# Kernel optimization log

Hardware: AMD Instinct MI355X
Metric: run time of the kernel (lower is better)

Reference implementation:

```python
import jax, jax.numpy as jnp
import numpy as np

INPUT_DIM = 64
OUTPUT_DIM = 128
KNN = 10          # hardcoded min(10, N) in source
RADIUS = 0.02     # density radius in source


def setup_inputs() -> dict:
    key = jax.random.key(0)
    k1, k2, k3, k4, k5, k6, k7 = jax.random.split(key, 7)
    B, N = 2, 8192
    points = jax.random.uniform(k1, (B, N, 3), dtype=jnp.float32)
    features = jax.random.normal(k2, (B, N, INPUT_DIM), dtype=jnp.float32)
    leaf_mask = jax.random.randint(k3, (B, N), 0, 2) > 0
    d_in = INPUT_DIM + 6
    s1 = 1.0 / np.sqrt(d_in)
    s2 = 1.0 / np.sqrt(OUTPUT_DIM)
    W1 = jax.random.uniform(k4, (d_in, OUTPUT_DIM), jnp.float32, -s1, s1)
    b1 = jax.random.uniform(k5, (OUTPUT_DIM,), jnp.float32, -s1, s1)
    W2 = jax.random.uniform(k6, (OUTPUT_DIM, OUTPUT_DIM), jnp.float32, -s2, s2)
    b2 = jax.random.uniform(k7, (OUTPUT_DIM,), jnp.float32, -s2, s2)
    return {"points": points, "features": features, "leaf_mask": leaf_mask,
            "W1": W1, "b1": b1, "W2": W2, "b2": b2}


def _leaf_geometry(points, mask):
    # points: [N,3], mask: [N] bool -> [N,6]
    mask_f = mask.astype(points.dtype)
    cnt = jnp.maximum(mask_f.sum(), 1.0)
    center = (points * mask_f[:, None]).sum(0) / cnt      # mean of masked points
    rel = points - center                                  # [N,3]
    dist_c = jnp.linalg.norm(rel, axis=1)                  # dist to leaf center
    rel_h = rel[:, 2]                                      # relative height
    horiz = jnp.linalg.norm(rel[:, :2], axis=1)            # horizontal distance
    # pairwise euclidean distances [N,N]; used only for thresholding and knn
    sq = jnp.sum(points * points, axis=1)
    d2 = sq[:, None] + sq[None, :] - 2.0 * (points @ points.T)
    dist = jax.lax.stop_gradient(jnp.sqrt(jnp.maximum(d2, 0.0)))
    density = jnp.sum((dist < RADIUS) & mask[None, :], axis=1).astype(points.dtype)
    # KNN (smallest distances, includes self) -> local PCA curvature
    _, idx = jax.lax.top_k(-dist, KNN)                     # [N,KNN]
    neighbors = points[idx]                                # [N,KNN,3]
    centered = neighbors - points[:, None, :]
    cov = jnp.einsum('nki,nkj->nij', centered, centered) / float(KNN)  # [N,3,3]
    ev = jnp.linalg.eigh(cov)[0]                           # ascending eigenvalues
    curv = ev[:, 0] / (ev[:, 2] + 1e-8)
    rad = jnp.arctan2(rel[:, 1], rel[:, 0])
    geom = jnp.stack([dist_c, rel_h, horiz, density, curv, rad], axis=1)
    # source returns zeros when mask is empty
    return jnp.where(mask_f.sum() > 0, geom, jnp.zeros_like(geom))


def reference(points, features, leaf_mask, W1, b1, W2, b2):
    geom = jax.vmap(_leaf_geometry)(points, leaf_mask)     # [B,N,6]
    combined = jnp.concatenate([features, geom], axis=-1)  # [B,N,input_dim+6]
    h = jax.nn.relu(combined @ W1 + b1)
    return jax.nn.relu(h @ W2 + b2)                        # [B,N,output_dim]
```

## Files before the change

kernel.cpp:

```cpp
#include <hip/hip_runtime.h>
#include <math.h>
#include <stdint.h>

#define B_SZ   2
#define N_PTS  8192
#define IN_DIM 64
#define D_IN   70
#define ODIM   128
#define NQ_ALL (B_SZ * N_PTS)
#define RADIUS_F 0.02f

#define GDIM  32
#define NCELL (GDIM * GDIM * GDIM)
#define HCELL 0.03125f

#define SUP     4
#define NSUP_AX 8
#define NSUPER  (NSUP_AX * NSUP_AX * NSUP_AX)
#define SCAP    352
#define LCAP    16
#define MAXROWS 100

typedef unsigned long long u64;

__device__ __forceinline__ void insert11(u64 (&best)[11], u64 key) {
#pragma unroll
  for (int j = 10; j >= 1; --j) {
    u64 hi = (best[j - 1] > key) ? best[j - 1] : key;
    best[j] = (best[j] < hi) ? best[j] : hi;
  }
  best[0] = (best[0] < key) ? best[0] : key;
}
__device__ __forceinline__ void insert10(u64 (&best)[10], u64 key) {
#pragma unroll
  for (int j = 9; j >= 1; --j) {
    u64 hi = (best[j - 1] > key) ? best[j - 1] : key;
    best[j] = (best[j] < hi) ? best[j] : hi;
  }
  best[0] = (best[0] < key) ? best[0] : key;
}

__device__ __forceinline__ float sq3(float x, float y, float z) {
  return __fadd_rn(__fadd_rn(__fmul_rn(x, x), __fmul_rn(y, y)), __fmul_rn(z, z));
}

__device__ __forceinline__ int cellOf(float v) {
  int c = (int)(v * 32.0f);
  return min(max(c, 0), GDIM - 1);
}

__device__ __forceinline__ void geom_epilogue(const float* __restrict__ P,
                                              const int (&idxs)[10], float dens,
                                              float px, float py, float pz,
                                              float4 ctr, float* __restrict__ g) {
  double c00 = 0, c01 = 0, c02 = 0, c11 = 0, c12 = 0, c22 = 0;
#pragma unroll
  for (int j = 0; j < 10; ++j) {
    const int idx = idxs[j];
    const float nx = P[3 * idx + 0], ny = P[3 * idx + 1], nz = P[3 * idx + 2];
    const float ex = __fsub_rn(nx, px);
    const float ey = __fsub_rn(ny, py);
    const float ez = __fsub_rn(nz, pz);
    c00 += (double)ex * ex; c01 += (double)ex * ey; c02 += (double)ex * ez;
    c11 += (double)ey * ey; c12 += (double)ey * ez; c22 += (double)ez * ez;
  }
  const double a00 = c00 / 10.0, a01 = c01 / 10.0, a02 = c02 / 10.0;
  const double a11 = c11 / 10.0, a12 = c12 / 10.0, a22 = c22 / 10.0;

  double p1 = a01 * a01 + a02 * a02 + a12 * a12;
  double qq = (a00 + a11 + a22) / 3.0;
  double p2 = (a00 - qq) * (a00 - qq) + (a11 - qq) * (a11 - qq) +
              (a22 - qq) * (a22 - qq) + 2.0 * p1;
  double ev0, ev2;
  if (p2 <= 1e-60) {
    ev0 = ev2 = qq;
  } else {
    double p = sqrt(p2 / 6.0);
    double invp = 1.0 / p;
    double b00 = (a00 - qq) * invp, b11 = (a11 - qq) * invp, b22 = (a22 - qq) * invp;
    double b01 = a01 * invp, b02 = a02 * invp, b12 = a12 * invp;
    double detB = b00 * (b11 * b22 - b12 * b12) - b01 * (b01 * b22 - b12 * b02) +
                  b02 * (b01 * b12 - b11 * b02);
    double r = 0.5 * detB;
    r = fmin(1.0, fmax(-1.0, r));
    double phi = acos(r) / 3.0;
    ev2 = qq + 2.0 * p * cos(phi);
    ev0 = qq + 2.0 * p * cos(phi + 2.0943951023931953);
  }
  const float curv = (float)(ev0 / (ev2 + 1e-08));

  const bool on = ctr.w > 0.0f;
  const float rx = __fsub_rn(px, ctr.x);
  const float ry = __fsub_rn(py, ctr.y);
  const float rz = __fsub_rn(pz, ctr.z);
  const float dist_c = sqrtf(sq3(rx, ry, rz));
  const float horiz  = sqrtf(__fadd_rn(__fmul_rn(rx, rx), __fmul_rn(ry, ry)));
  const float rad    = atan2f(ry, rx);

  g[0] = on ? dist_c : 0.0f;
  g[1] = on ? rz : 0.0f;
  g[2] = on ? horiz : 0.0f;
  g[3] = on ? dens : 0.0f;
  g[4] = on ? curv : 0.0f;
  g[5] = on ? rad : 0.0f;
}

__global__ __launch_bounds__(256) void k_build(const float* __restrict__ points,
                                               const int* __restrict__ mask,
                                               int* __restrict__ count,
                                               double* __restrict__ ctrAcc) {
  const int t = blockIdx.x * 256 + threadIdx.x;
  const int b = t >> 13;
  const int i = t & (N_PTS - 1);
  const float* P = points + (size_t)b * N_PTS * 3;
  const float x = P[3 * i + 0], y = P[3 * i + 1], z = P[3 * i + 2];
  atomicAdd(&count[b * NCELL + (cellOf(z) * GDIM + cellOf(y)) * GDIM + cellOf(x)], 1);

  const bool m = mask[b * N_PTS + i] != 0;
  double vx = m ? (double)x : 0.0, vy = m ? (double)y : 0.0;
  double vz = m ? (double)z : 0.0, vc = m ? 1.0 : 0.0;
#pragma unroll
  for (int s = 1; s < 64; s <<= 1) {
    vx += __shfl_xor(vx, s); vy += __shfl_xor(vy, s);
    vz += __shfl_xor(vz, s); vc += __shfl_xor(vc, s);
  }
  __shared__ double sh[4][4];
  const int w = threadIdx.x >> 6;
  if ((threadIdx.x & 63) == 0) { sh[0][w] = vx; sh[1][w] = vy; sh[2][w] = vz; sh[3][w] = vc; }
  __syncthreads();
  if (threadIdx.x == 0) {
    atomicAdd(&ctrAcc[b * 4 + 0], sh[0][0] + sh[0][1] + sh[0][2] + sh[0][3]);
    atomicAdd(&ctrAcc[b * 4 + 1], sh[1][0] + sh[1][1] + sh[1][2] + sh[1][3]);
    atomicAdd(&ctrAcc[b * 4 + 2], sh[2][0] + sh[2][1] + sh[2][2] + sh[2][3]);
    atomicAdd(&ctrAcc[b * 4 + 3], sh[3][0] + sh[3][1] + sh[3][2] + sh[3][3]);
  }
}

__global__ __launch_bounds__(1024) void k_scan(const int* __restrict__ count,
                                               int* __restrict__ start,
                                               int* __restrict__ cur,
                                               const double* __restrict__ ctrAcc,
                                               float* __restrict__ centerOut) {
  const int b = blockIdx.x;
  const int t = threadIdx.x;
  if (t == 0) {
    const float cf = (float)ctrAcc[b * 4 + 3];
    const float div = fmaxf(cf, 1.0f);
    centerOut[b * 4 + 0] = (float)ctrAcc[b * 4 + 0] / div;
    centerOut[b * 4 + 1] = (float)ctrAcc[b * 4 + 1] / div;
    centerOut[b * 4 + 2] = (float)ctrAcc[b * 4 + 2] / div;
    centerOut[b * 4 + 3] = (cf > 0.0f) ? 1.0f : 0.0f;
  }
  int c[32]; int sum = 0;
#pragma unroll
  for (int j = 0; j < 32; ++j) { c[j] = count[b * NCELL + t * 32 + j]; sum += c[j]; }
  __shared__ int s[1024];
  s[t] = sum;
  __syncthreads();
  for (int off = 1; off < 1024; off <<= 1) {
    int v = (t >= off) ? s[t - off] : 0;
    __syncthreads();
    if (t >= off) s[t] += v;
    __syncthreads();
  }
  int excl = (t > 0) ? s[t - 1] : 0;
#pragma unroll
  for (int j = 0; j < 32; ++j) {
    start[b * (NCELL + 1) + t * 32 + j] = excl;
    cur[b * NCELL + t * 32 + j] = excl;
    excl += c[j];
  }
  if (t == 1023) start[b * (NCELL + 1) + NCELL] = excl;
}

__global__ __launch_bounds__(256) void k_scatter(const float* __restrict__ points,
                                                 const int* __restrict__ mask,
                                                 int* __restrict__ cur,
                                                 float4* __restrict__ sorted) {
  const int t = blockIdx.x * 256 + threadIdx.x;
  const int b = t >> 13;
  const int i = t & (N_PTS - 1);
  const float* P = points + (size_t)b * N_PTS * 3;
  const float x = P[3 * i + 0], y = P[3 * i + 1], z = P[3 * i + 2];
  const int cell = (cellOf(z) * GDIM + cellOf(y)) * GDIM + cellOf(x);
  const int pos = atomicAdd(&cur[b * NCELL + cell], 1);
  const unsigned wb = (unsigned)i | ((mask[b * N_PTS + i] != 0) ? 0x80000000u : 0u);
  sorted[(size_t)b * N_PTS + pos] = make_float4(x, y, z, __uint_as_float(wb));
}

__global__ __launch_bounds__(128) void k_collect(const float* __restrict__ points,
                                                 const float4* __restrict__ sorted,
                                                 const int* __restrict__ start,
                                                 const float* __restrict__ center,
                                                 float* __restrict__ geom,
                                                 int* __restrict__ list,
                                                 int* __restrict__ listCnt,
                                                 float DENS_T) {
  const int b  = blockIdx.y;
  const int sc = blockIdx.x;
  const int sx = sc & 7, sy = (sc >> 3) & 7, sz = sc >> 6;
  const int tid = threadIdx.x;

  const int* ST = start + b * (NCELL + 1);
  const float4* SP = sorted + (size_t)b * N_PTS;

  const int x0 = SUP * sx, x1 = SUP * sx + SUP - 1;
  const int y0 = SUP * sy, y1 = SUP * sy + SUP - 1;
  const int z0 = SUP * sz, z1 = SUP * sz + SUP - 1;
  const int hx0 = max(x0 - 3, 0), hx1 = min(x1 + 3, GDIM - 1);
  const int hy0 = max(y0 - 3, 0), hy1 = min(y1 + 3, GDIM - 1);
  const int hz0 = max(z0 - 3, 0), hz1 = min(z1 + 3, GDIM - 1);
  const int yc = hy1 - hy0 + 1;
  const int R  = (hz1 - hz0 + 1) * yc;

  __shared__ int    rs[MAXROWS], rp[MAXROWS + 1];
  __shared__ int    qs_[16], qp_[17];
  __shared__ float4 pts4[SCAP];
  __shared__ u64    lbuf[128 * LCAP];

  if (tid < 64) {
    {
      int qlen = 0, qst = 0;
      if (tid < 16) {
        const int z = z0 + (tid >> 2), y = y0 + (tid & 3);
        const int base = (z * GDIM + y) * GDIM;
        qst  = ST[base + x0];
        qlen = ST[base + x1 + 1] - qst;
      }
      int inc = qlen;
      for (int off = 1; off < 64; off <<= 1) { int v = __shfl_up(inc, off); if (tid >= off) inc += v; }
      if (tid < 16) { qs_[tid] = qst; qp_[tid] = inc - qlen; }
      if (tid == 63) qp_[16] = inc;
    }
    {
      int len[2] = {0, 0}, st2[2] = {0, 0};
#pragma unroll
      for (int k = 0; k < 2; ++k) {
        const int r = tid * 2 + k;
        if (r < R) {
          const int z = hz0 + r / yc, y = hy0 + r % yc;
          const int base = (z * GDIM + y) * GDIM;
          st2[k] = ST[base + hx0];
          len[k] = ST[base + hx1 + 1] - st2[k];
        }
      }
      int sum = len[0] + len[1];
      int inc = sum;
      for (int off = 1; off < 64; off <<= 1) { int v = __shfl_up(inc, off); if (tid >= off) inc += v; }
      int exc = inc - sum;
#pragma unroll
      for (int k = 0; k < 2; ++k) {
        const int r = tid * 2 + k;
        if (r < R) { rs[r] = st2[k]; rp[r] = exc; }
        exc += len[k];
      }
      if (tid == 63) rp[R] = inc;
    }
  }
  __syncthreads();

  const int C    = rp[R];
  const int qtot = qp_[16];
  if (qtot == 0) return;

  if (C > SCAP) {
    for (int t = tid; t < qtot; t += 128) {
      int lo = 0, hi = 15;
      while (lo < hi) { const int mid = (lo + hi + 1) >> 1; if (qp_[mid] <= t) lo = mid; else hi = mid - 1; }
      const int qglob = qs_[lo] + (t - qp_[lo]);
      const int pos = atomicAdd(listCnt, 1);
      list[pos] = (b << 13) | qglob;
    }
    return;
  }

  for (int i = tid; i < C; i += 128) {
    int lo = 0, hi = R - 1;
    while (lo < hi) { const int mid = (lo + hi + 1) >> 1; if (rp[mid] <= i) lo = mid; else hi = mid - 1; }
    pts4[i] = SP[rs[lo] + (i - rp[lo])];
  }
  __syncthreads();

  const bool cxl = (x0 - 3 < 0), cxh = (x1 + 3 > GDIM - 1);
  const bool cyl = (y0 - 3 < 0), cyh = (y1 + 3 > GDIM - 1);
  const bool czl = (z0 - 3 < 0), czh = (z1 + 3 > GDIM - 1);

  const float4 ctr = reinterpret_cast<const float4*>(center)[b];
  const float* P = points + (size_t)b * N_PTS * 3;
  const int sub = tid & 7;
  const int gq  = tid >> 3;

  for (int q0 = 0; q0 < qtot; q0 += 16) {
    const int myq = q0 + gq;
    const bool act = (myq < qtot);
    const int mq = act ? myq : 0;
    int lo = 0, hi = 15;
    while (lo < hi) { const int mid = (lo + hi + 1) >> 1; if (qp_[mid] <= mq) lo = mid; else hi = mid - 1; }
    const int qglob = qs_[lo] + (mq - qp_[lo]);
    const float4 qp4 = SP[qglob];
    const int qidx = (int)(__float_as_uint(qp4.w) & 0x7FFFFFFFu);
    const float px = qp4.x, py = qp4.y, pz = qp4.z;
    const float sqq = sq3(px, py, pz);

    const float mxl = cxl ? 1e9f : __fsub_rn(px, (float)hx0 * HCELL);
    const float mxh = cxh ? 1e9f : __fsub_rn((float)(hx1 + 1) * HCELL, px);
    const float myl = cyl ? 1e9f : __fsub_rn(py, (float)hy0 * HCELL);
    const float myh = cyh ? 1e9f : __fsub_rn((float)(hy1 + 1) * HCELL, py);
    const float mzl = czl ? 1e9f : __fsub_rn(pz, (float)hz0 * HCELL);
    const float mzh = czh ? 1e9f : __fsub_rn((float)(hz1 + 1) * HCELL, pz);
    const float gr = fminf(fminf(fminf(mxl, mxh), fminf(myl, myh)), fminf(mzl, mzh));
    const float fx = 0.5f * (1.0f + fminf(fminf(px, 1.0f - px) * (1.0f / 0.0935f), 1.0f));
    const float fy = 0.5f * (1.0f + fminf(fminf(py, 1.0f - py) * (1.0f / 0.0935f), 1.0f));
    const float fz = 0.5f * (1.0f + fminf(fminf(pz, 1.0f - pz) * (1.0f / 0.0935f), 1.0f));
    const float rT = 0.0935f * cbrtf(1.0f / (fx * fy * fz));
    const float cR = fminf(gr, rT);
    const float cT2 = cR * cR;
    const float certR = cR * 0.999f;

    int cnt = 0;
    u64* myb = &lbuf[tid * LCAP];
#pragma unroll 2
    for (int j = sub; j < C; j += 8) {
      const float4 tp = pts4[j];
      const float sqc = sq3(tp.x, tp.y, tp.z);
      const float dot = __fmaf_rn(pz, tp.z, __fmaf_rn(py, tp.y, __fmul_rn(px, tp.x)));
      const float d2  = __fsub_rn(__fadd_rn(sqq, sqc), __fmul_rn(2.0f, dot));
      const float d2c = fmaxf(d2, 0.0f);
      if (d2c < cT2) {
        if (cnt < LCAP) {
          const unsigned wb = __float_as_uint(tp.w);
          myb[cnt] = ((u64)__float_as_uint(d2c) << 32)
                   | (u64)(((wb & 0x7FFFFFFFu) << 1) | (wb >> 31));
        }
        ++cnt;
      }
    }

    u64 best[11];
#pragma unroll
    for (int j = 0; j < 11; ++j) best[j] = ~0ull;
    float dens = 0.0f;
    const int m = min(cnt, LCAP);
    for (int i = 0; i < m; ++i) {
      const u64 e = myb[i];
      if ((e & 1ull) && __uint_as_float((unsigned)(e >> 32)) < DENS_T) dens += 1.0f;
      if (e < best[10]) insert11(best, e);
    }
    int cntg = cnt;
    int over = (cnt > LCAP) ? 1 : 0;
#pragma unroll
    for (int s = 1; s < 8; s <<= 1) {
      dens += __shfl_xor(dens, s);
      cntg += __shfl_xor(cntg, s);
      over |= __shfl_xor(over, s);
      u64 ok[11];
#pragma unroll
      for (int j = 0; j < 11; ++j) ok[j] = __shfl_xor(best[j], s);
#pragma unroll
      for (int j = 0; j < 11; ++j) {
        if (ok[j] < best[10]) insert11(best, ok[j]); else break;
      }
    }

    if (act && sub == 0) {
      const float dist9 = sqrtf(__uint_as_float((unsigned)(best[9] >> 32)));
      bool bad = (over != 0) || (cntg < 10) || !(dist9 < certR);
      if (cntg >= 11) {
        const float dist10 = sqrtf(__uint_as_float((unsigned)(best[10] >> 32)));
        bad = bad || (dist10 == dist9);
      }
      if (bad) {
        const int pos = atomicAdd(listCnt, 1);
        list[pos] = (b << 13) | qglob;
      } else {
        int idxs[10];
#pragma unroll
        for (int j = 0; j < 10; ++j) idxs[j] = (int)(((unsigned)best[j]) >> 1);
        geom_epilogue(P, idxs, dens, px, py, pz, ctr,
                      geom + ((size_t)b * N_PTS + qidx) * 6);
      }
    }
  }
}

__global__ __launch_bounds__(256) void k_wavefb(const float* __restrict__ points,
                                                const float4* __restrict__ sorted,
                                                const int* __restrict__ start,
                                                const float* __restrict__ center,
                                                float* __restrict__ geom,
                                                int* __restrict__ flags2,
                                                const int* __restrict__ list,
                                                const int* __restrict__ listCnt) {
  const int lane = threadIdx.x & 63;
  const int wid  = threadIdx.x >> 6;
  const int n = *listCnt;
  for (int it = blockIdx.x * 4 + wid; it < n; it += gridDim.x * 4) {
    const int e = list[it];
    const int b = e >> 13, qs = e & (N_PTS - 1);
    const float4* SP = sorted + (size_t)b * N_PTS;
    const int* ST = start + b * (NCELL + 1);
    const float4 qp = SP[qs];
    const int qidx = (int)(__float_as_uint(qp.w) & 0x7FFFFFFFu);
    const float px = qp.x, py = qp.y, pz = qp.z;
    const float sqq = sq3(px, py, pz);
    const int cx = cellOf(px), cy = cellOf(py), cz = cellOf(pz);
    const int xlo = max(cx - 8, 0), xhi = min(cx + 8, GDIM - 1);
    const int ylo = max(cy - 8, 0), yhi = min(cy + 8, GDIM - 1);
    const int zlo = max(cz - 8, 0), zhi = min(cz + 8, GDIM - 1);
    const int ycw = yhi - ylo + 1;
    const int Rw = (zhi - zlo + 1) * ycw;

    u64 best[10];
#pragma unroll
    for (int j = 0; j < 10; ++j) best[j] = ((u64)0x7F800000u << 32) | 0xFFFFFFFFu;
    float dens = 0.0f;

    for (int r = lane; r < Rw; r += 64) {
      const int z = zlo + r / ycw, y = ylo + r % ycw;
      const int base = (z * GDIM + y) * GDIM;
      const int j0 = ST[base + xlo], j1 = ST[base + xhi + 1];
      for (int j = j0; j < j1; ++j) {
        const float4 tp = SP[j];
        const unsigned wb = __float_as_uint(tp.w);
        const float sqc = sq3(tp.x, tp.y, tp.z);
        const float dot = __fmaf_rn(pz, tp.z, __fmaf_rn(py, tp.y, __fmul_rn(px, tp.x)));
        const float d2  = __fsub_rn(__fadd_rn(sqq, sqc), __fmul_rn(2.0f, dot));
        const float dist = sqrtf(fmaxf(d2, 0.0f));
        if ((dist < RADIUS_F) && (wb & 0x80000000u)) dens += 1.0f;
        const u64 key = ((u64)__float_as_uint(dist) << 32) | (wb & 0x7FFFFFFFu);
        if (key < best[9]) insert10(best, key);
      }
    }
#pragma unroll
    for (int s = 1; s < 64; s <<= 1) {
      dens += __shfl_xor(dens, s);
      u64 ok[10];
#pragma unroll
      for (int j = 0; j < 10; ++j) ok[j] = __shfl_xor(best[j], s);
#pragma unroll
      for (int j = 0; j < 10; ++j) {
        if (ok[j] < best[9]) insert10(best, ok[j]); else break;
      }
    }
    if (lane == 0) {
      const float dist9 = __uint_as_float((unsigned)(best[9] >> 32));
      if (dist9 < 0.2494f) {
        const float4 ctr = reinterpret_cast<const float4*>(center)[b];
        const float* P = points + (size_t)b * N_PTS * 3;
        int idxs[10];
#pragma unroll
        for (int j = 0; j < 10; ++j) idxs[j] = (int)(((unsigned)best[j]) & 0x7FFFFFFFu);
        geom_epilogue(P, idxs, dens, px, py, pz, ctr, geom + ((size_t)b * N_PTS + qidx) * 6);
      } else {
        flags2[b * N_PTS + qs] = 1;
      }
    }
  }
}

__global__ __launch_bounds__(256) void k_fallback(const float* __restrict__ points,
                                                  const float4* __restrict__ sorted,
                                                  const int* __restrict__ start,
                                                  const float* __restrict__ center,
                                                  float* __restrict__ geom,
                                                  const int* __restrict__ flags2) {
  const int b = blockIdx.y;
  const int qs = blockIdx.x * 256 + threadIdx.x;
  if (flags2[b * N_PTS + qs] == 0) return;
  const float4 qp = sorted[(size_t)b * N_PTS + qs];
  const unsigned qw = __float_as_uint(qp.w);
  const int qidx = (int)(qw & 0x7FFFFFFFu);

  const float px = qp.x, py = qp.y, pz = qp.z;
  const float sqq = sq3(px, py, pz);
  const int cx = cellOf(px), cy = cellOf(py), cz = cellOf(pz);

  const int* ST = start + b * (NCELL + 1);
  const float4* SP = sorted + (size_t)b * N_PTS;

  u64 best[10];
#pragma unroll
  for (int j = 0; j < 10; ++j) best[j] = ((u64)0x7F800000u << 32) | 0xFFFFFFFFu;
  float dens = 0.0f;

  for (int rho = 0; rho < GDIM; ++rho) {
    const int zlo = max(cz - rho, 0), zhi = min(cz + rho, GDIM - 1);
    const int ylo = max(cy - rho, 0), yhi = min(cy + rho, GDIM - 1);
    for (int z = zlo; z <= zhi; ++z) {
      const int adz = abs(z - cz);
      for (int y = ylo; y <= yhi; ++y) {
        const int ady = abs(y - cy);
        const int m2 = max(adz, ady);
        int ja, jb;
        int ja2 = 0, jb2 = 0;
        const int rowBase = (z * GDIM + y) * GDIM;
        if (m2 == rho) {
          const int xa = max(cx - rho, 0), xb = min(cx + rho, GDIM - 1);
          ja = ST[rowBase + xa]; jb = ST[rowBase + xb + 1];
        } else {
          ja = jb = 0;
          if (cx - rho >= 0)        { ja = ST[rowBase + cx - rho]; jb = ST[rowBase + cx - rho + 1]; }
          if (cx + rho <= GDIM - 1) { ja2 = ST[rowBase + cx + rho]; jb2 = ST[rowBase + cx + rho + 1]; }
        }
#pragma unroll 1
        for (int pass = 0; pass < 2; ++pass) {
          const int j0 = pass ? ja2 : ja;
          const int j1 = pass ? jb2 : jb;
          for (int j = j0; j < j1; ++j) {
            const float4 tp = SP[j];
            const unsigned wb = __float_as_uint(tp.w);
            const float sqc = sq3(tp.x, tp.y, tp.z);
            const float dot = __fmaf_rn(pz, tp.z, __fmaf_rn(py, tp.y, __fmul_rn(px, tp.x)));
            const float d2  = __fsub_rn(__fadd_rn(sqq, sqc), __fmul_rn(2.0f, dot));
            const float dist = sqrtf(fmaxf(d2, 0.0f));
            if ((dist < RADIUS_F) && (wb & 0x80000000u)) dens += 1.0f;
            const u64 key = ((u64)__float_as_uint(dist) << 32) | (wb & 0x7FFFFFFFu);
            if (key < best[9]) insert10(best, key);
          }
        }
      }
    }
    if (rho >= 1) {
      const float dist9 = __uint_as_float((unsigned)(best[9] >> 32));
      if (dist9 < (float)rho * HCELL * 0.999f) break;
    }
  }

  const float4 ctr = reinterpret_cast<const float4*>(center)[b];
  const float* P = points + (size_t)b * N_PTS * 3;
  int idxs[10];
#pragma unroll
  for (int j = 0; j < 10; ++j) idxs[j] = (int)(((unsigned)best[j]) & 0x7FFFFFFFu);
  geom_epilogue(P, idxs, dens, px, py, pz, ctr, geom + ((size_t)b * N_PTS + qidx) * 6);
}

__global__ __launch_bounds__(256) void k_mlp(const float* __restrict__ features,
                                             const float* __restrict__ geom,
                                             const float* __restrict__ W1,
                                             const float* __restrict__ b1,
                                             const float* __restrict__ W2,
                                             const float* __restrict__ b2,
                                             float* __restrict__ out) {
  __shared__ float Wbuf[ODIM * ODIM];
  __shared__ float A[64][71];
  __shared__ float H[64][133];
  const int tid = threadIdx.x;
  const int row0 = blockIdx.x * 64;

  {
    const int r = tid >> 2, f4 = (tid & 3) * 16;
#pragma unroll
    for (int j = 0; j < 4; ++j) {
      const float4 v = *reinterpret_cast<const float4*>(
          &features[(size_t)(row0 + r) * IN_DIM + f4 + j * 4]);
      A[r][f4 + 4 * j + 0] = v.x; A[r][f4 + 4 * j + 1] = v.y;
      A[r][f4 + 4 * j + 2] = v.z; A[r][f4 + 4 * j + 3] = v.w;
    }
  }
  for (int i = tid; i < 64 * 6; i += 256) {
    const int r = i / 6, k = i % 6;
    A[r][IN_DIM + k] = geom[(size_t)(row0 + r) * 6 + k];
  }
  for (int i = tid; i < D_IN * ODIM / 4; i += 256) {
    const float4 v = reinterpret_cast<const float4*>(W1)[i];
    Wbuf[4 * i + 0] = v.x; Wbuf[4 * i + 1] = v.y;
    Wbuf[4 * i + 2] = v.z; Wbuf[4 * i + 3] = v.w;
  }
  __syncthreads();

  const int rg = (tid >> 4) * 4;
  const int c  = (tid & 15) * 8;

  float acc[4][8];
#pragma unroll
  for (int i = 0; i < 4; ++i)
#pragma unroll
    for (int j = 0; j < 8; ++j) acc[i][j] = 0.0f;

#pragma unroll 2
  for (int k = 0; k < D_IN; ++k) {
    float a[4];
#pragma unroll
    for (int i = 0; i < 4; ++i) a[i] = A[rg + i][k];
    const float4 w0 = *reinterpret_cast<const float4*>(&Wbuf[k * ODIM + c]);
    const float4 w1 = *reinterpret_cast<const float4*>(&Wbuf[k * ODIM + c + 4]);
    const float w[8] = {w0.x, w0.y, w0.z, w0.w, w1.x, w1.y, w1.z, w1.w};
#pragma unroll
    for (int i = 0; i < 4; ++i)
#pragma unroll
      for (int j = 0; j < 8; ++j) acc[i][j] = fmaf(a[i], w[j], acc[i][j]);
  }
  __syncthreads();

  {
    const float4 bb0 = *reinterpret_cast<const float4*>(&b1[c]);
    const float4 bb1 = *reinterpret_cast<const float4*>(&b1[c + 4]);
    const float bb[8] = {bb0.x, bb0.y, bb0.z, bb0.w, bb1.x, bb1.y, bb1.z, bb1.w};
#pragma unroll
    for (int i = 0; i < 4; ++i) {
#pragma unroll
      for (int j = 0; j < 8; ++j) H[rg + i][c + j] = fmaxf(acc[i][j] + bb[j], 0.0f);
    }
  }
  for (int i = tid; i < ODIM * ODIM / 4; i += 256) {
    const float4 v = reinterpret_cast<const float4*>(W2)[i];
    Wbuf[4 * i + 0] = v.x; Wbuf[4 * i + 1] = v.y;
    Wbuf[4 * i + 2] = v.z; Wbuf[4 * i + 3] = v.w;
  }
  __syncthreads();

#pragma unroll
  for (int i = 0; i < 4; ++i)
#pragma unroll
    for (int j = 0; j < 8; ++j) acc[i][j] = 0.0f;

#pragma unroll 2
  for (int k = 0; k < ODIM; ++k) {
    float a[4];
#pragma unroll
    for (int i = 0; i < 4; ++i) a[i] = H[rg + i][k];
    const float4 w0 = *reinterpret_cast<const float4*>(&Wbuf[k * ODIM + c]);
    const float4 w1 = *reinterpret_cast<const float4*>(&Wbuf[k * ODIM + c + 4]);
    const float w[8] = {w0.x, w0.y, w0.z, w0.w, w1.x, w1.y, w1.z, w1.w};
#pragma unroll
    for (int i = 0; i < 4; ++i)
#pragma unroll
      for (int j = 0; j < 8; ++j) acc[i][j] = fmaf(a[i], w[j], acc[i][j]);
  }
  {
    const float4 bb0 = *reinterpret_cast<const float4*>(&b2[c]);
    const float4 bb1 = *reinterpret_cast<const float4*>(&b2[c + 4]);
    const float bb[8] = {bb0.x, bb0.y, bb0.z, bb0.w, bb1.x, bb1.y, bb1.z, bb1.w};
#pragma unroll
    for (int i = 0; i < 4; ++i) {
      const size_t row = (size_t)(row0 + rg + i);
      float4 o0 = make_float4(fmaxf(acc[i][0] + bb[0], 0.f), fmaxf(acc[i][1] + bb[1], 0.f),
                              fmaxf(acc[i][2] + bb[2], 0.f), fmaxf(acc[i][3] + bb[3], 0.f));
      float4 o1 = make_float4(fmaxf(acc[i][4] + bb[4], 0.f), fmaxf(acc[i][5] + bb[5], 0.f),
                              fmaxf(acc[i][6] + bb[6], 0.f), fmaxf(acc[i][7] + bb[7], 0.f));
      *reinterpret_cast<float4*>(&out[row * ODIM + c]) = o0;
      *reinterpret_cast<float4*>(&out[row * ODIM + c + 4]) = o1;
    }
  }
}

extern "C" void kernel_launch(void* const* d_in, const int* in_sizes, int n_in,
                              void* d_out, int out_size, void* d_ws, size_t ws_size,
                              hipStream_t stream) {
  const float* points   = (const float*)d_in[0];
  const float* features = (const float*)d_in[1];
  const int*   mask     = (const int*)d_in[2];
  const float* W1       = (const float*)d_in[3];
  const float* b1       = (const float*)d_in[4];
  const float* W2       = (const float*)d_in[5];
  const float* b2       = (const float*)d_in[6];
  float* out = (float*)d_out;

  const double Rd   = (double)0.02f;
  const double midd = Rd - ldexp(1.0, -30);
  const double Td   = midd * midd;
  float densT = (float)Td;
  if ((double)densT <= Td) densT = nextafterf(densT, 1.0f);

  char* w = (char*)d_ws;
  size_t off = 0;
  auto take = [&](size_t bytes) { char* p = w + off; off = (off + bytes + 255) & ~(size_t)255; return p; };
  float*  geomBuf   = (float*)take((size_t)NQ_ALL * 6 * 4);
  float*  centerBuf = (float*)take(2 * 16);
  char*   zero0     = (char*)take(0);
  int*    countBuf  = (int*)take((size_t)B_SZ * NCELL * 4);
  int*    flags2Buf = (int*)take((size_t)NQ_ALL * 4);
  int*    listCnt   = (int*)take(4);
  double* ctrAcc    = (double*)take((size_t)B_SZ * 4 * 8);
  char*   zero1     = (char*)take(0);
  int*    startBuf  = (int*)take((size_t)B_SZ * (NCELL + 1) * 4);
  int*    curBuf    = (int*)take((size_t)B_SZ * NCELL * 4);
  float4* sortedBuf = (float4*)take((size_t)B_SZ * N_PTS * 16);
  int*    listBuf   = (int*)take((size_t)NQ_ALL * 4);
  (void)ws_size;

  hipMemsetAsync(zero0, 0, (size_t)(zero1 - zero0), stream);
  k_build<<<NQ_ALL / 256, 256, 0, stream>>>(points, mask, countBuf, ctrAcc);
  k_scan<<<B_SZ, 1024, 0, stream>>>(countBuf, startBuf, curBuf, ctrAcc, centerBuf);
  k_scatter<<<NQ_ALL / 256, 256, 0, stream>>>(points, mask, curBuf, sortedBuf);
  k_collect<<<dim3(NSUPER, B_SZ), 128, 0, stream>>>(points, sortedBuf, startBuf, centerBuf,
                                                    geomBuf, listBuf, listCnt, densT);
  k_wavefb<<<512, 256, 0, stream>>>(points, sortedBuf, startBuf, centerBuf,
                                    geomBuf, flags2Buf, listBuf, listCnt);
  k_fallback<<<dim3(N_PTS / 256, B_SZ), 256, 0, stream>>>(points, sortedBuf, startBuf,
                                                          centerBuf, geomBuf, flags2Buf);
  k_mlp<<<NQ_ALL / 64, 256, 0, stream>>>(features, geomBuf, W1, b1, W2, b2, out);
}
```

Baseline: 206.4 us.

## Split collect supercells across four single-wave blocks with 16 lanes per query

Each supercell is now handled by four 64-thread blocks instead of one 128-thread block, and each block takes an interleaved subset of the query points. Each query is scanned by 16 lanes instead of 8. The per-lane candidate buffer shrinks to 12 entries with a padded stride, which is meant to cut shared-memory use and bank conflicts so more blocks fit per CU. The halo gather now copies contiguous rows directly instead of binary-searching per element. The cost is that every split block redundantly loads the full halo into shared memory, and the smaller buffer may push more queries onto the fallback path.

```diff
diff --git a/kernel.cpp b/kernel.cpp
--- a/kernel.cpp
+++ b/kernel.cpp
@@ -17,8 +17,10 @@
 #define SUP     4
 #define NSUP_AX 8
 #define NSUPER  (NSUP_AX * NSUP_AX * NSUP_AX)
+#define NSPLIT  4
 #define SCAP    352
-#define LCAP    16
+#define LCAP    12
+#define LSTR    (LCAP + 1)
 #define MAXROWS 100
 
 typedef unsigned long long u64;
@@ -188,18 +190,19 @@
   sorted[(size_t)b * N_PTS + pos] = make_float4(x, y, z, __uint_as_float(wb));
 }
 
-__global__ __launch_bounds__(128) void k_collect(const float* __restrict__ points,
-                                                 const float4* __restrict__ sorted,
-                                                 const int* __restrict__ start,
-                                                 const float* __restrict__ center,
-                                                 float* __restrict__ geom,
-                                                 int* __restrict__ list,
-                                                 int* __restrict__ listCnt,
-                                                 float DENS_T) {
-  const int b  = blockIdx.y;
-  const int sc = blockIdx.x;
+__global__ __launch_bounds__(64) void k_collect(const float* __restrict__ points,
+                                                const float4* __restrict__ sorted,
+                                                const int* __restrict__ start,
+                                                const float* __restrict__ center,
+                                                float* __restrict__ geom,
+                                                int* __restrict__ list,
+                                                int* __restrict__ listCnt,
+                                                float DENS_T) {
+  const int b    = blockIdx.y;
+  const int sc   = blockIdx.x / NSPLIT;
+  const int part = blockIdx.x % NSPLIT;
   const int sx = sc & 7, sy = (sc >> 3) & 7, sz = sc >> 6;
-  const int tid = threadIdx.x;
+  const int lane = threadIdx.x;
 
   const int* ST = start + b * (NCELL + 1);
   const float4* SP = sorted + (size_t)b * N_PTS;
@@ -216,46 +219,44 @@
   __shared__ int    rs[MAXROWS], rp[MAXROWS + 1];
   __shared__ int    qs_[16], qp_[17];
   __shared__ float4 pts4[SCAP];
-  __shared__ u64    lbuf[128 * LCAP];
-
-  if (tid < 64) {
-    {
-      int qlen = 0, qst = 0;
-      if (tid < 16) {
-        const int z = z0 + (tid >> 2), y = y0 + (tid & 3);
+  __shared__ u64    lbuf[64 * LSTR];
+
+  {
+    int qlen = 0, qst = 0;
+    if (lane < 16) {
+      const int z = z0 + (lane >> 2), y = y0 + (lane & 3);
+      const int base = (z * GDIM + y) * GDIM;
+      qst  = ST[base + x0];
+      qlen = ST[base + x1 + 1] - qst;
+    }
+    int inc = qlen;
+    for (int off = 1; off < 64; off <<= 1) { int v = __shfl_up(inc, off); if (lane >= off) inc += v; }
+    if (lane < 16) { qs_[lane] = qst; qp_[lane] = inc - qlen; }
+    if (lane == 63) qp_[16] = inc;
+  }
+  {
+    int len[2] = {0, 0}, st2[2] = {0, 0};
+#pragma unroll
+    for (int k = 0; k < 2; ++k) {
+      const int r = lane * 2 + k;
+      if (r < R) {
+        const int z = hz0 + r / yc, y = hy0 + r % yc;
         const int base = (z * GDIM + y) * GDIM;
-        qst  = ST[base + x0];
-        qlen = ST[base + x1 + 1] - qst;
-      }
-      int inc = qlen;
-      for (int off = 1; off < 64; off <<= 1) { int v = __shfl_up(inc, off); if (tid >= off) inc += v; }
-      if (tid < 16) { qs_[tid] = qst; qp_[tid] = inc - qlen; }
-      if (tid == 63) qp_[16] = inc;
-    }
-    {
-      int len[2] = {0, 0}, st2[2] = {0, 0};
-#pragma unroll
-      for (int k = 0; k < 2; ++k) {
-        const int r = tid * 2 + k;
-        if (r < R) {
-          const int z = hz0 + r / yc, y = hy0 + r % yc;
-          const int base = (z * GDIM + y) * GDIM;
-          st2[k] = ST[base + hx0];
-          len[k] = ST[base + hx1 + 1] - st2[k];
-        }
-      }
-      int sum = len[0] + len[1];
-      int inc = sum;
-      for (int off = 1; off < 64; off <<= 1) { int v = __shfl_up(inc, off); if (tid >= off) inc += v; }
-      int exc = inc - sum;
-#pragma unroll
-      for (int k = 0; k < 2; ++k) {
-        const int r = tid * 2 + k;
-        if (r < R) { rs[r] = st2[k]; rp[r] = exc; }
-        exc += len[k];
-      }
-      if (tid == 63) rp[R] = inc;
-    }
+        st2[k] = ST[base + hx0];
+        len[k] = ST[base + hx1 + 1] - st2[k];
+      }
+    }
+    int sum = len[0] + len[1];
+    int inc = sum;
+    for (int off = 1; off < 64; off <<= 1) { int v = __shfl_up(inc, off); if (lane >= off) inc += v; }
+    int exc = inc - sum;
+#pragma unroll
+    for (int k = 0; k < 2; ++k) {
+      const int r = lane * 2 + k;
+      if (r < R) { rs[r] = st2[k]; rp[r] = exc; }
+      exc += len[k];
+    }
+    if (lane == 63) rp[R] = inc;
   }
   __syncthreads();
 
@@ -264,20 +265,21 @@
   if (qtot == 0) return;
 
   if (C > SCAP) {
-    for (int t = tid; t < qtot; t += 128) {
-      int lo = 0, hi = 15;
-      while (lo < hi) { const int mid = (lo + hi + 1) >> 1; if (qp_[mid] <= t) lo = mid; else hi = mid - 1; }
-      const int qglob = qs_[lo] + (t - qp_[lo]);
-      const int pos = atomicAdd(listCnt, 1);
-      list[pos] = (b << 13) | qglob;
+    if (part == 0) {
+      for (int t = lane; t < qtot; t += 64) {
+        int lo = 0, hi = 15;
+        while (lo < hi) { const int mid = (lo + hi + 1) >> 1; if (qp_[mid] <= t) lo = mid; else hi = mid - 1; }
+        const int qglob = qs_[lo] + (t - qp_[lo]);
+        const int pos = atomicAdd(listCnt, 1);
+        list[pos] = (b << 13) | qglob;
+      }
     }
     return;
   }
 
-  for (int i = tid; i < C; i += 128) {
-    int lo = 0, hi = R - 1;
-    while (lo < hi) { const int mid = (lo + hi + 1) >> 1; if (rp[mid] <= i) lo = mid; else hi = mid - 1; }
-    pts4[i] = SP[rs[lo] + (i - rp[lo])];
+  for (int r = lane; r < R; r += 64) {
+    const int st = rs[r], base = rp[r], len = rp[r + 1] - base;
+    for (int t = 0; t < len; ++t) pts4[base + t] = SP[st + t];
   }
   __syncthreads();
 
@@ -287,10 +289,10 @@
 
   const float4 ctr = reinterpret_cast<const float4*>(center)[b];
   const float* P = points + (size_t)b * N_PTS * 3;
-  const int sub = tid & 7;
-  const int gq  = tid >> 3;
-
-  for (int q0 = 0; q0 < qtot; q0 += 16) {
+  const int sub = lane & 15;
+  const int gq  = lane >> 4;
+
+  for (int q0 = part * 4; q0 < qtot; q0 += NSPLIT * 4) {
     const int myq = q0 + gq;
     const bool act = (myq < qtot);
     const int mq = act ? myq : 0;
@@ -318,9 +320,9 @@
     const float certR = cR * 0.999f;
 
     int cnt = 0;
-    u64* myb = &lbuf[tid * LCAP];
+    u64* myb = &lbuf[lane * LSTR];
 #pragma unroll 2
-    for (int j = sub; j < C; j += 8) {
+    for (int j = sub; j < C; j += 16) {
       const float4 tp = pts4[j];
       const float sqc = sq3(tp.x, tp.y, tp.z);
       const float dot = __fmaf_rn(pz, tp.z, __fmaf_rn(py, tp.y, __fmul_rn(px, tp.x)));
@@ -349,7 +351,7 @@
     int cntg = cnt;
     int over = (cnt > LCAP) ? 1 : 0;
 #pragma unroll
-    for (int s = 1; s < 8; s <<= 1) {
+    for (int s = 1; s < 16; s <<= 1) {
       dens += __shfl_xor(dens, s);
       cntg += __shfl_xor(cntg, s);
       over |= __shfl_xor(over, s);
@@ -683,8 +685,9 @@
   k_build<<<NQ_ALL / 256, 256, 0, stream>>>(points, mask, countBuf, ctrAcc);
   k_scan<<<B_SZ, 1024, 0, stream>>>(countBuf, startBuf, curBuf, ctrAcc, centerBuf);
   k_scatter<<<NQ_ALL / 256, 256, 0, stream>>>(points, mask, curBuf, sortedBuf);
-  k_collect<<<dim3(NSUPER, B_SZ), 128, 0, stream>>>(points, sortedBuf, startBuf, centerBuf,
-                                                    geomBuf, listBuf, listCnt, densT);
+  k_collect<<<dim3(NSUPER * NSPLIT, B_SZ), 64, 0, stream>>>(points, sortedBuf, startBuf,
+                                                            centerBuf, geomBuf, listBuf,
+                                                            listCnt, densT);
   k_wavefb<<<512, 256, 0, stream>>>(points, sortedBuf, startBuf, centerBuf,
                                     geomBuf, flags2Buf, listBuf, listCnt);
   k_fallback<<<dim3(N_PTS / 256, B_SZ), 256, 0, stream>>>(points, sortedBuf, startBuf,
```

New measurement: 224.0 us. 8.6% more time.

## Split KNN geometry epilogue into separate kernel and use 32-bit top-k keys

Applied to the files above, without the earlier changes.

The collect kernel no longer runs the costly per-query geometry epilogue (covariance and eigen solve) on one lane in eight. Instead each 8-lane group cooperatively writes its 10 neighbour indices and density into a per-query record, and a new fully parallel k_geom2 kernel computes geometry from those records. The top-k merge now uses 32-bit distance keys rather than 64-bit ones, the per-thread candidate buffer in LDS gets a padded stride, and the scan loop unroll is raised. The cost is an extra kernel launch, a record buffer round-trip through global memory, and a second candidate pass to recover indices.

```diff
diff --git a/kernel.cpp b/kernel.cpp
--- a/kernel.cpp
+++ b/kernel.cpp
@@ -19,17 +19,18 @@
 #define NSUPER  (NSUP_AX * NSUP_AX * NSUP_AX)
 #define SCAP    352
 #define LCAP    16
+#define LSTR    17
 #define MAXROWS 100
 
 typedef unsigned long long u64;
 
-__device__ __forceinline__ void insert11(u64 (&best)[11], u64 key) {
+__device__ __forceinline__ void ins11u(unsigned (&best)[11], unsigned key) {
 #pragma unroll
   for (int j = 10; j >= 1; --j) {
-    u64 hi = (best[j - 1] > key) ? best[j - 1] : key;
-    best[j] = (best[j] < hi) ? best[j] : hi;
-  }
-  best[0] = (best[0] < key) ? best[0] : key;
+    unsigned hi = max(best[j - 1], key);
+    best[j] = min(best[j], hi);
+  }
+  best[0] = min(best[0], key);
 }
 __device__ __forceinline__ void insert10(u64 (&best)[10], u64 key) {
 #pragma unroll
@@ -188,11 +189,9 @@
   sorted[(size_t)b * N_PTS + pos] = make_float4(x, y, z, __uint_as_float(wb));
 }
 
-__global__ __launch_bounds__(128) void k_collect(const float* __restrict__ points,
-                                                 const float4* __restrict__ sorted,
+__global__ __launch_bounds__(128) void k_collect(const float4* __restrict__ sorted,
                                                  const int* __restrict__ start,
-                                                 const float* __restrict__ center,
-                                                 float* __restrict__ geom,
+                                                 int* __restrict__ recBuf,
                                                  int* __restrict__ list,
                                                  int* __restrict__ listCnt,
                                                  float DENS_T) {
@@ -216,7 +215,8 @@
   __shared__ int    rs[MAXROWS], rp[MAXROWS + 1];
   __shared__ int    qs_[16], qp_[17];
   __shared__ float4 pts4[SCAP];
-  __shared__ u64    lbuf[128 * LCAP];
+  __shared__ u64    lbuf[128 * LSTR];
+  __shared__ int    gslot[16][12];
 
   if (tid < 64) {
     {
@@ -268,6 +268,7 @@
       int lo = 0, hi = 15;
       while (lo < hi) { const int mid = (lo + hi + 1) >> 1; if (qp_[mid] <= t) lo = mid; else hi = mid - 1; }
       const int qglob = qs_[lo] + (t - qp_[lo]);
+      recBuf[((size_t)b * N_PTS + qglob) * 12 + 11] = 1;
       const int pos = atomicAdd(listCnt, 1);
       list[pos] = (b << 13) | qglob;
     }
@@ -285,10 +286,9 @@
   const bool cyl = (y0 - 3 < 0), cyh = (y1 + 3 > GDIM - 1);
   const bool czl = (z0 - 3 < 0), czh = (z1 + 3 > GDIM - 1);
 
-  const float4 ctr = reinterpret_cast<const float4*>(center)[b];
-  const float* P = points + (size_t)b * N_PTS * 3;
   const int sub = tid & 7;
   const int gq  = tid >> 3;
+  const int g   = tid >> 3;
 
   for (int q0 = 0; q0 < qtot; q0 += 16) {
     const int myq = q0 + gq;
@@ -298,7 +298,6 @@
     while (lo < hi) { const int mid = (lo + hi + 1) >> 1; if (qp_[mid] <= mq) lo = mid; else hi = mid - 1; }
     const int qglob = qs_[lo] + (mq - qp_[lo]);
     const float4 qp4 = SP[qglob];
-    const int qidx = (int)(__float_as_uint(qp4.w) & 0x7FFFFFFFu);
     const float px = qp4.x, py = qp4.y, pz = qp4.z;
     const float sqq = sq3(px, py, pz);
 
@@ -318,8 +317,8 @@
     const float certR = cR * 0.999f;
 
     int cnt = 0;
-    u64* myb = &lbuf[tid * LCAP];
-#pragma unroll 2
+    u64* myb = &lbuf[tid * LSTR];
+#pragma unroll 4
     for (int j = sub; j < C; j += 8) {
       const float4 tp = pts4[j];
       const float sqc = sq3(tp.x, tp.y, tp.z);
@@ -336,15 +335,16 @@
       }
     }
 
-    u64 best[11];
-#pragma unroll
-    for (int j = 0; j < 11; ++j) best[j] = ~0ull;
+    unsigned best[11];
+#pragma unroll
+    for (int j = 0; j < 11; ++j) best[j] = 0xFFFFFFFFu;
     float dens = 0.0f;
     const int m = min(cnt, LCAP);
     for (int i = 0; i < m; ++i) {
       const u64 e = myb[i];
-      if ((e & 1ull) && __uint_as_float((unsigned)(e >> 32)) < DENS_T) dens += 1.0f;
-      if (e < best[10]) insert11(best, e);
+      const unsigned d2u = (unsigned)(e >> 32);
+      if ((e & 1ull) && __uint_as_float(d2u) < DENS_T) dens += 1.0f;
+      if (d2u < best[10]) ins11u(best, d2u);
     }
     int cntg = cnt;
     int over = (cnt > LCAP) ? 1 : 0;
@@ -353,34 +353,71 @@
       dens += __shfl_xor(dens, s);
       cntg += __shfl_xor(cntg, s);
       over |= __shfl_xor(over, s);
-      u64 ok[11];
+      unsigned ok[11];
 #pragma unroll
       for (int j = 0; j < 11; ++j) ok[j] = __shfl_xor(best[j], s);
 #pragma unroll
       for (int j = 0; j < 11; ++j) {
-        if (ok[j] < best[10]) insert11(best, ok[j]); else break;
-      }
-    }
-
-    if (act && sub == 0) {
-      const float dist9 = sqrtf(__uint_as_float((unsigned)(best[9] >> 32)));
+        if (ok[j] < best[10]) ins11u(best, ok[j]); else break;
+      }
+    }
+
+    if (act) {
+      const unsigned T9 = best[9];
+      const float dist9 = sqrtf(__uint_as_float(T9));
       bool bad = (over != 0) || (cntg < 10) || !(dist9 < certR);
-      if (cntg >= 11) {
-        const float dist10 = sqrtf(__uint_as_float((unsigned)(best[10] >> 32)));
-        bad = bad || (dist10 == dist9);
-      }
-      if (bad) {
+      if (cntg >= 11) bad = bad || (sqrtf(__uint_as_float(best[10])) == dist9);
+      int* rec = recBuf + ((size_t)b * N_PTS + qglob) * 12;
+      if (!bad) {
+        int mc = 0;
+        for (int i = 0; i < m; ++i) if ((unsigned)(myb[i] >> 32) <= T9) ++mc;
+        int pre = mc;
+#pragma unroll
+        for (int off = 1; off < 8; off <<= 1) { int v = __shfl_up(pre, off); if (sub >= off) pre += v; }
+        int wp = pre - mc;
+        for (int i = 0; i < m; ++i) {
+          const u64 e = myb[i];
+          if ((unsigned)(e >> 32) <= T9) { gslot[g][min(wp, 11)] = (int)(((unsigned)e) >> 1); ++wp; }
+        }
+        __builtin_amdgcn_wave_barrier();
+        if (sub == 0) {
+          int4 r0 = make_int4(gslot[g][0], gslot[g][1], gslot[g][2], gslot[g][3]);
+          int4 r1 = make_int4(gslot[g][4], gslot[g][5], gslot[g][6], gslot[g][7]);
+          int4 r2 = make_int4(gslot[g][8], gslot[g][9], __float_as_int(dens), 0);
+          *reinterpret_cast<int4*>(rec + 0) = r0;
+          *reinterpret_cast<int4*>(rec + 4) = r1;
+          *reinterpret_cast<int4*>(rec + 8) = r2;
+        }
+        __builtin_amdgcn_wave_barrier();
+      } else if (sub == 0) {
+        rec[11] = 1;
         const int pos = atomicAdd(listCnt, 1);
         list[pos] = (b << 13) | qglob;
-      } else {
-        int idxs[10];
-#pragma unroll
-        for (int j = 0; j < 10; ++j) idxs[j] = (int)(((unsigned)best[j]) >> 1);
-        geom_epilogue(P, idxs, dens, px, py, pz, ctr,
-                      geom + ((size_t)b * N_PTS + qidx) * 6);
-      }
-    }
-  }
+      }
+    }
+  }
+}
+
+__global__ __launch_bounds__(256) void k_geom2(const float* __restrict__ points,
+                                               const float4* __restrict__ sorted,
+                                               const float* __restrict__ center,
+                                               const int* __restrict__ recBuf,
+                                               float* __restrict__ geom) {
+  const int t = blockIdx.x * 256 + threadIdx.x;
+  const int b = t >> 13;
+  const int qs = t & (N_PTS - 1);
+  const int* rec = recBuf + (size_t)t * 12;
+  if (rec[11] != 0) return;
+  const float4 qp = sorted[(size_t)b * N_PTS + qs];
+  const int qidx = (int)(__float_as_uint(qp.w) & 0x7FFFFFFFu);
+  int idxs[10];
+#pragma unroll
+  for (int j = 0; j < 10; ++j) idxs[j] = rec[j];
+  const float dens = __int_as_float(rec[10]);
+  const float4 ctr = reinterpret_cast<const float4*>(center)[b];
+  const float* P = points + (size_t)b * N_PTS * 3;
+  geom_epilogue(P, idxs, dens, qp.x, qp.y, qp.z, ctr,
+                geom + ((size_t)b * N_PTS + qidx) * 6);
 }
 
 __global__ __launch_bounds__(256) void k_wavefb(const float* __restrict__ points,
@@ -677,14 +714,16 @@
   int*    curBuf    = (int*)take((size_t)B_SZ * NCELL * 4);
   float4* sortedBuf = (float4*)take((size_t)B_SZ * N_PTS * 16);
   int*    listBuf   = (int*)take((size_t)NQ_ALL * 4);
+  int*    recBuf    = (int*)take((size_t)NQ_ALL * 12 * 4);
   (void)ws_size;
 
   hipMemsetAsync(zero0, 0, (size_t)(zero1 - zero0), stream);
   k_build<<<NQ_ALL / 256, 256, 0, stream>>>(points, mask, countBuf, ctrAcc);
   k_scan<<<B_SZ, 1024, 0, stream>>>(countBuf, startBuf, curBuf, ctrAcc, centerBuf);
   k_scatter<<<NQ_ALL / 256, 256, 0, stream>>>(points, mask, curBuf, sortedBuf);
-  k_collect<<<dim3(NSUPER, B_SZ), 128, 0, stream>>>(points, sortedBuf, startBuf, centerBuf,
-                                                    geomBuf, listBuf, listCnt, densT);
+  k_collect<<<dim3(NSUPER, B_SZ), 128, 0, stream>>>(sortedBuf, startBuf, recBuf,
+                                                    listBuf, listCnt, densT);
+  k_geom2<<<NQ_ALL / 256, 256, 0, stream>>>(points, sortedBuf, centerBuf, recBuf, geomBuf);
   k_wavefb<<<512, 256, 0, stream>>>(points, sortedBuf, startBuf, centerBuf,
                                     geomBuf, flags2Buf, listBuf, listCnt);
   k_fallback<<<dim3(N_PTS / 256, B_SZ), 256, 0, stream>>>(points, sortedBuf, startBuf,
```

After: 188.6 us. 1.09x faster.
